# Kernel tuning notes

Hardware: AMD Instinct MI355X
Metric: run time of the kernel (lower is better)

The kernel has to match this reference:

```python
import jax, jax.numpy as jnp
import numpy as np

FEATURES = 4096
BATCH = 2048


def setup_inputs() -> dict:
    key = jax.random.key(0)
    kx, kk = jax.random.split(key)
    x = jax.random.normal(kx, (BATCH, FEATURES), dtype=jnp.float32)
    kernel = jax.random.normal(kk, (FEATURES,), dtype=jnp.float32)
    return {"x": x, "kernel": kernel}


def reference(x, kernel):
    n = kernel.shape[0]
    i = jnp.arange(n)[:, None]   # [n,1]
    j = jnp.arange(n)[None, :]   # [1,n]
    idx = i - j                   # Toeplitz offsets
    # W[i,j] = kernel[i-j] if i>=j else 0  (causal lower-triangular Toeplitz)
    W = jnp.where(idx >= 0, kernel[jnp.clip(idx, 0, n - 1)], 0.0)
    # out[b,i] = sum_{j<=i} x[b,j] * kernel[i-j]  == x @ W.T
    return x @ W.T
```

## Files before the change

kernel.cpp:

```cpp
#include <hip/hip_runtime.h>
#include <hip/hip_bf16.h>


typedef unsigned short u16;
typedef __attribute__((ext_vector_type(8))) short  bf16x8;
typedef __attribute__((ext_vector_type(8))) unsigned short u16x8;
typedef __attribute__((ext_vector_type(4))) float  f32x4;

#define KDIM 4096
#define NDIM 4096
#define MDIM 2048
#define KREV_STRIDE 4608
#define KREV_BYTES  (8 * KREV_STRIDE * 2)

#define MFMA_BF16 __builtin_amdgcn_mfma_f32_16x16x32_bf16

static __device__ inline u16 f2bf(float f) {
  unsigned u = __builtin_bit_cast(unsigned, f);
  unsigned r = u + 0x7FFFu + ((u >> 16) & 1u);
  return (u16)(r >> 16);
}

static __device__ inline void async_copy16(const void* g, void* l) {
  __builtin_amdgcn_global_load_lds((const __attribute__((address_space(1))) void*)g,
                                   (__attribute__((address_space(3))) void*)l,
                                   16, 0, 0);
}

__global__ __launch_bounds__(256) void prep(const float* __restrict__ x,
                                            const float* __restrict__ kern,
                                            u16* __restrict__ xb,
                                            u16* __restrict__ krevs,
                                            int conv_blocks) {
  int kblk = (int)blockIdx.x - conv_blocks;
  if (kblk >= 0) {
    int u = kblk * 256 + threadIdx.x;
    for (int a = 0; a < 8; ++a) {
      int t = u + a - 8;
      u16 v = 0;
      if (t >= 0 && t <= 4095) v = f2bf(kern[4095 - t]);
      krevs[a * KREV_STRIDE + u] = v;
    }
  } else {
    unsigned tg  = blockIdx.x * 256 + threadIdx.x;
    unsigned l   = tg & 63;
    unsigned kb  = (tg >> 6) & 127;
    unsigned rg  = tg >> 13;
    unsigned row = rg * 16 + (l & 15);
    unsigned k   = kb * 32 + (l >> 4) * 8;
    const f32x4* p = (const f32x4*)(x + (size_t)row * KDIM + k);
    f32x4 v0 = p[0], v1 = p[1];
    u16x8 r;
    r[0] = f2bf(v0[0]); r[1] = f2bf(v0[1]); r[2] = f2bf(v0[2]); r[3] = f2bf(v0[3]);
    r[4] = f2bf(v1[0]); r[5] = f2bf(v1[1]); r[6] = f2bf(v1[2]); r[7] = f2bf(v1[3]);
    *(u16x8*)(xb + (size_t)tg * 8) = r;
  }
}

template <bool CONV>
__global__ __launch_bounds__(512, 4) void toeplitz_gemm(const void* __restrict__ Av,
                                                        const u16* __restrict__ krevs,
                                                        float* __restrict__ out) {
  __shared__ __align__(16) char smem_raw[69888];
  u16*   B_all = (u16*)smem_raw;
  f32x4* ep    = (f32x4*)smem_raw;

  const int tid  = threadIdx.x;
  const int w    = tid >> 6;
  const int g    = w >> 2;
  const int wl   = w & 3;
  const int lane = tid & 63;
  const int lane16 = lane & 15;
  const int quad   = lane >> 4;
  const int wm = wl >> 1;
  const int wn = wl & 1;

  const int b   = (int)blockIdx.x;
  const int x_  = b & 7;
  const int jj  = b >> 3;
  const int p_  = x_ + 8 * (jj & 1);
  const int ctp = (jj >> 1) & 15;
  const int cn  = jj >> 5;
  const int ct1 = 31 - ctp;
  const int ct2 = ctp;
  const int m0  = p_ * 128;

  const int stride1 = 128 * (ct1 + 1) + 72;
  const int stride2 = 128 * (ct2 + 1) + 72;
  const int base2   = 8 * stride1;
  const int W1 = 4032 - (ct1 * 128 + cn * 64);
  const int W2 = 4032 - (ct2 * 128 + cn * 64);

  const int wmu = __builtin_amdgcn_readfirstlane(wm);
  const int gu  = __builtin_amdgcn_readfirstlane(g);
  const u16*   xb2 = (const u16*)Av;
  const float* xf  = (const float*)Av;
  int aoffs[4];
  for (int fm = 0; fm < 4; ++fm)
    aoffs[fm] = (p_ * 8 + wmu * 4 + fm) * 65536 + gu * 1024 + lane * 8;
  const int rowb = m0 + wm * 64 + lane16;

  auto ldA = [&](int fm, int t, int kk) -> bf16x8 {
    return *(const bf16x8*)(xb2 + aoffs[fm] + t * 2048 + kk * 512);
  };
  auto ldAc = [&](int fm, int t, int kk) -> bf16x8 {
    const float* px = xf + (size_t)(rowb + fm * 16) * KDIM +
                      t * 128 + gu * 64 + kk * 32 + quad * 8;
    f32x4 v0 = *(const f32x4*)px, v1 = *(const f32x4*)(px + 4);
    u16x8 r;
    r[0]=f2bf(v0[0]); r[1]=f2bf(v0[1]); r[2]=f2bf(v0[2]); r[3]=f2bf(v0[3]);
    r[4]=f2bf(v1[0]); r[5]=f2bf(v1[1]); r[6]=f2bf(v1[2]); r[7]=f2bf(v1[3]);
    return __builtin_bit_cast(bf16x8, r);
  };

  auto stageWin = [&](int base_e, int stride_e, int Wp) {
    const u16* src = krevs + w * KREV_STRIDE + Wp;
    char* dstb = smem_raw + (size_t)(base_e + w * stride_e) * 2;
    for (int c = 0; c * 512 < stride_e; ++c) {
      int idx = c * 512 + lane * 8;
      if (idx < stride_e)
        async_copy16(src + idx, dstb + (size_t)c * 1024);
    }
  };
  stageWin(0, stride1, W1);
  stageWin(base2, stride2, W2);
  asm volatile("s_waitcnt vmcnt(0)" ::: "memory");
  __builtin_amdgcn_s_barrier();
  asm volatile("" ::: "memory");

  auto runPhase = [&](int ctq, int base_e, int stride_q, int Wq) {
    const int n0c = ctq * 128 + cn * 64;
    int boff[2];
    for (int fn = 0; fn < 2; ++fn) {
      int n_g = n0c + wn * 32 + fn * 16 + lane16;
      int s0  = 4095 - n_g + quad * 8;
      int a   = s0 & 7;
      boff[fn] = base_e + a * stride_q + (s0 - a + 8 - Wq);
    }
    f32x4 acc[4][2] = {};

    if constexpr (!CONV) {
      bf16x8 afA[4], afB[4];
#pragma unroll
      for (int fm = 0; fm < 4; ++fm) afA[fm] = ldA(fm, 0, 0);
#pragma unroll
      for (int fm = 0; fm < 4; ++fm) afB[fm] = ldA(fm, 0, 1);
      for (int t = 0; ; ++t) {
        const int ks = t * 128 + g * 64;
#pragma unroll
        for (int fn = 0; fn < 2; ++fn) {
          bf16x8 bv = *(const bf16x8*)(&B_all[boff[fn] + ks]);
#pragma unroll
          for (int fm = 0; fm < 4; ++fm)
            acc[fm][fn] = MFMA_BF16(afA[fm], bv, acc[fm][fn], 0, 0, 0);
        }
        if (t < ctq)
#pragma unroll
          for (int fm = 0; fm < 4; ++fm) afA[fm] = ldA(fm, t + 1, 0);
#pragma unroll
        for (int fn = 0; fn < 2; ++fn) {
          bf16x8 bv = *(const bf16x8*)(&B_all[boff[fn] + ks + 32]);
#pragma unroll
          for (int fm = 0; fm < 4; ++fm)
            acc[fm][fn] = MFMA_BF16(afB[fm], bv, acc[fm][fn], 0, 0, 0);
        }
        if (t == ctq) break;
#pragma unroll
        for (int fm = 0; fm < 4; ++fm) afB[fm] = ldA(fm, t + 1, 1);
      }
    } else {
      for (int t = 0; t <= ctq; ++t) {
        const int ks = t * 128 + g * 64;
#pragma unroll
        for (int kk = 0; kk < 2; ++kk) {
          bf16x8 af[4];
#pragma unroll
          for (int fm = 0; fm < 4; ++fm) af[fm] = ldAc(fm, t, kk);
#pragma unroll
          for (int fn = 0; fn < 2; ++fn) {
            bf16x8 bv = *(const bf16x8*)(&B_all[boff[fn] + ks + kk * 32]);
#pragma unroll
            for (int fm = 0; fm < 4; ++fm)
              acc[fm][fn] = MFMA_BF16(af[fm], bv, acc[fm][fn], 0, 0, 0);
          }
        }
      }
    }

    const int j = tid & 255;
    __syncthreads();
#pragma unroll
    for (int r = 0; r < 2; ++r) {
      if (r) __syncthreads();
      if (g == 1) {
        for (int fm2 = 0; fm2 < 2; ++fm2)
          for (int fn = 0; fn < 2; ++fn)
            ep[j * 5 + fm2 * 2 + fn] = acc[r * 2 + fm2][fn];
      }
      __syncthreads();
      if (g == 0) {
        for (int fm2 = 0; fm2 < 2; ++fm2)
          for (int fn = 0; fn < 2; ++fn) {
            f32x4 v = acc[r * 2 + fm2][fn];
            f32x4 o = ep[j * 5 + fm2 * 2 + fn];
            v[0] += o[0]; v[1] += o[1]; v[2] += o[2]; v[3] += o[3];
            int fm = r * 2 + fm2;
            int row_base = m0 + wm * 64 + fm * 16 + quad * 4;
            int col = n0c + wn * 32 + fn * 16 + lane16;
            for (int rr = 0; rr < 4; ++rr)
              out[(size_t)(row_base + rr) * NDIM + col] = v[rr];
          }
      }
    }
  };

  runPhase(ct1, 0, stride1, W1);
  runPhase(ct2, base2, stride2, W2);
}

extern "C" void kernel_launch(void* const* d_in, const int* in_sizes, int n_in,
                              void* d_out, int out_size, void* d_ws, size_t ws_size,
                              hipStream_t stream) {
  const float* x    = (const float*)d_in[0];
  const float* kern = (const float*)d_in[1];
  float* out = (float*)d_out;

  u16* krevs = (u16*)d_ws;
  u16* xb    = (u16*)((char*)d_ws + KREV_BYTES);
  const size_t need_fast = (size_t)KREV_BYTES + (size_t)MDIM * KDIM * 2;

  if (ws_size >= need_fast) {
    prep<<<4096 + 18, 256, 0, stream>>>(x, kern, xb, krevs, 4096);
    toeplitz_gemm<false><<<512, 512, 0, stream>>>(xb, krevs, out);
  } else {
    prep<<<18, 256, 0, stream>>>(x, kern, xb, krevs, 0);
    toeplitz_gemm<true><<<512, 512, 0, stream>>>(x, krevs, out);
  }
}
```

Measured before the change: 123.9 us.

## Widen block N tile to 128 columns and double-buffer B fragments

Each block now covers a full 128-column tile instead of 64, so the grid halves to 256 blocks. Each wave holds 4x4 accumulators, which doubles the MFMA work per A fragment load and improves A reuse. The B fragments from LDS are prefetched into registers a k-step ahead, and the LDS window and epilogue staging grow to match. In exchange, register pressure rises (launch bounds drop to 2 blocks per SM) and there are fewer blocks, which risks lower occupancy and tail imbalance on 256 CUs.

```diff
diff --git a/kernel.cpp b/kernel.cpp
--- a/kernel.cpp
+++ b/kernel.cpp
@@ -58,10 +58,10 @@
 }
 
 template <bool CONV>
-__global__ __launch_bounds__(512, 4) void toeplitz_gemm(const void* __restrict__ Av,
+__global__ __launch_bounds__(512, 2) void toeplitz_gemm(const void* __restrict__ Av,
                                                         const u16* __restrict__ krevs,
                                                         float* __restrict__ out) {
-  __shared__ __align__(16) char smem_raw[69888];
+  __shared__ __align__(16) char smem_raw[73984];
   u16*   B_all = (u16*)smem_raw;
   f32x4* ep    = (f32x4*)smem_raw;
 
@@ -79,17 +79,16 @@
   const int x_  = b & 7;
   const int jj  = b >> 3;
   const int p_  = x_ + 8 * (jj & 1);
-  const int ctp = (jj >> 1) & 15;
-  const int cn  = jj >> 5;
+  const int ctp = jj >> 1;
   const int ct1 = 31 - ctp;
   const int ct2 = ctp;
   const int m0  = p_ * 128;
 
-  const int stride1 = 128 * (ct1 + 1) + 72;
-  const int stride2 = 128 * (ct2 + 1) + 72;
+  const int stride1 = 128 * (ct1 + 1) + 200;
+  const int stride2 = 128 * (ct2 + 1) + 200;
   const int base2   = 8 * stride1;
-  const int W1 = 4032 - (ct1 * 128 + cn * 64);
-  const int W2 = 4032 - (ct2 * 128 + cn * 64);
+  const int W1 = 3968 - 128 * ct1;
+  const int W2 = 3968 - 128 * ct2;
 
   const int wmu = __builtin_amdgcn_readfirstlane(wm);
   const int gu  = __builtin_amdgcn_readfirstlane(g);
@@ -129,41 +128,47 @@
   asm volatile("" ::: "memory");
 
   auto runPhase = [&](int ctq, int base_e, int stride_q, int Wq) {
-    const int n0c = ctq * 128 + cn * 64;
-    int boff[2];
-    for (int fn = 0; fn < 2; ++fn) {
-      int n_g = n0c + wn * 32 + fn * 16 + lane16;
+    const int n0q = ctq * 128;
+    int boff[4];
+    for (int fn = 0; fn < 4; ++fn) {
+      int n_g = n0q + wn * 64 + fn * 16 + lane16;
       int s0  = 4095 - n_g + quad * 8;
       int a   = s0 & 7;
       boff[fn] = base_e + a * stride_q + (s0 - a + 8 - Wq);
     }
-    f32x4 acc[4][2] = {};
+    f32x4 acc[4][4] = {};
 
     if constexpr (!CONV) {
-      bf16x8 afA[4], afB[4];
+      bf16x8 afA[4], afB[4], bvA[4], bvB[4];
 #pragma unroll
       for (int fm = 0; fm < 4; ++fm) afA[fm] = ldA(fm, 0, 0);
 #pragma unroll
       for (int fm = 0; fm < 4; ++fm) afB[fm] = ldA(fm, 0, 1);
+#pragma unroll
+      for (int fn = 0; fn < 4; ++fn)
+        bvA[fn] = *(const bf16x8*)(&B_all[boff[fn] + g * 64]);
       for (int t = 0; ; ++t) {
         const int ks = t * 128 + g * 64;
 #pragma unroll
-        for (int fn = 0; fn < 2; ++fn) {
-          bf16x8 bv = *(const bf16x8*)(&B_all[boff[fn] + ks]);
+        for (int fn = 0; fn < 4; ++fn)
+          bvB[fn] = *(const bf16x8*)(&B_all[boff[fn] + ks + 32]);
+#pragma unroll
+        for (int fn = 0; fn < 4; ++fn)
 #pragma unroll
           for (int fm = 0; fm < 4; ++fm)
-            acc[fm][fn] = MFMA_BF16(afA[fm], bv, acc[fm][fn], 0, 0, 0);
-        }
+            acc[fm][fn] = MFMA_BF16(afA[fm], bvA[fn], acc[fm][fn], 0, 0, 0);
         if (t < ctq)
 #pragma unroll
           for (int fm = 0; fm < 4; ++fm) afA[fm] = ldA(fm, t + 1, 0);
-#pragma unroll
-        for (int fn = 0; fn < 2; ++fn) {
-          bf16x8 bv = *(const bf16x8*)(&B_all[boff[fn] + ks + 32]);
+        if (t < ctq)
+#pragma unroll
+          for (int fn = 0; fn < 4; ++fn)
+            bvA[fn] = *(const bf16x8*)(&B_all[boff[fn] + ks + 128]);
+#pragma unroll
+        for (int fn = 0; fn < 4; ++fn)
 #pragma unroll
           for (int fm = 0; fm < 4; ++fm)
-            acc[fm][fn] = MFMA_BF16(afB[fm], bv, acc[fm][fn], 0, 0, 0);
-        }
+            acc[fm][fn] = MFMA_BF16(afB[fm], bvB[fn], acc[fm][fn], 0, 0, 0);
         if (t == ctq) break;
 #pragma unroll
         for (int fm = 0; fm < 4; ++fm) afB[fm] = ldA(fm, t + 1, 1);
@@ -177,7 +182,7 @@
 #pragma unroll
           for (int fm = 0; fm < 4; ++fm) af[fm] = ldAc(fm, t, kk);
 #pragma unroll
-          for (int fn = 0; fn < 2; ++fn) {
+          for (int fn = 0; fn < 4; ++fn) {
             bf16x8 bv = *(const bf16x8*)(&B_all[boff[fn] + ks + kk * 32]);
 #pragma unroll
             for (int fm = 0; fm < 4; ++fm)
@@ -188,25 +193,24 @@
     }
 
     const int j = tid & 255;
-    __syncthreads();
 #pragma unroll
     for (int r = 0; r < 2; ++r) {
-      if (r) __syncthreads();
+      __syncthreads();
       if (g == 1) {
         for (int fm2 = 0; fm2 < 2; ++fm2)
-          for (int fn = 0; fn < 2; ++fn)
-            ep[j * 5 + fm2 * 2 + fn] = acc[r * 2 + fm2][fn];
+          for (int fn = 0; fn < 4; ++fn)
+            ep[j * 9 + fm2 * 4 + fn] = acc[r * 2 + fm2][fn];
       }
       __syncthreads();
       if (g == 0) {
         for (int fm2 = 0; fm2 < 2; ++fm2)
-          for (int fn = 0; fn < 2; ++fn) {
+          for (int fn = 0; fn < 4; ++fn) {
             f32x4 v = acc[r * 2 + fm2][fn];
-            f32x4 o = ep[j * 5 + fm2 * 2 + fn];
+            f32x4 o = ep[j * 9 + fm2 * 4 + fn];
             v[0] += o[0]; v[1] += o[1]; v[2] += o[2]; v[3] += o[3];
             int fm = r * 2 + fm2;
             int row_base = m0 + wm * 64 + fm * 16 + quad * 4;
-            int col = n0c + wn * 32 + fn * 16 + lane16;
+            int col = n0q + wn * 64 + fn * 16 + lane16;
             for (int rr = 0; rr < 4; ++rr)
               out[(size_t)(row_base + rr) * NDIM + col] = v[rr];
           }
@@ -231,9 +235,9 @@
 
   if (ws_size >= need_fast) {
     prep<<<4096 + 18, 256, 0, stream>>>(x, kern, xb, krevs, 4096);
-    toeplitz_gemm<false><<<512, 512, 0, stream>>>(xb, krevs, out);
+    toeplitz_gemm<false><<<256, 512, 0, stream>>>(xb, krevs, out);
   } else {
     prep<<<18, 256, 0, stream>>>(x, kern, xb, krevs, 0);
-    toeplitz_gemm<true><<<512, 512, 0, stream>>>(x, krevs, out);
+    toeplitz_gemm<true><<<256, 512, 0, stream>>>(x, krevs, out);
   }
 }
```

After: 114.0 us. 8.0% less time.
